# Kernel optimization log

Measured on AMD Instinct MI355X. Metric: run time of the kernel, lower is better.

The kernel has to match this reference:

```python
import jax, jax.numpy as jnp
import numpy as np

EMBED_DIM = 512

def _equalized_linear(x, W):
    # StyleGAN equalized LR: effective weight = W / sqrt(fan_in); out = x @ W_eff.T
    c = 1.0 / np.sqrt(W.shape[1])
    return jnp.einsum('bnd,ed->bne', x, W) * c

def setup_inputs() -> dict:
    key = jax.random.key(0)
    ks = jax.random.split(key, 6)
    B, N, D = 16, 2048, 512
    return {
        'q': jax.random.normal(ks[0], (B, N, D), dtype=jnp.float32),
        'k': jax.random.normal(ks[1], (B, N, D), dtype=jnp.float32),
        'v': jax.random.normal(ks[2], (B, N, D), dtype=jnp.float32),
        'Wq': jax.random.normal(ks[3], (EMBED_DIM, D), dtype=jnp.float32),
        'Wk': jax.random.normal(ks[4], (EMBED_DIM, D), dtype=jnp.float32),
        'Wv': jax.random.normal(ks[5], (EMBED_DIM, D), dtype=jnp.float32),
    }

def reference(q, k, v, Wq, Wk, Wv):
    scale = EMBED_DIM ** (-0.5)
    qp = _equalized_linear(q, Wq)  # [B,Nq,E]
    kp = _equalized_linear(k, Wk)  # [B,Nk,E]
    vp = _equalized_linear(v, Wv)  # [B,Nk,E]
    dots = jnp.einsum('bqe,bke->bqk', qp, kp) * scale  # [B,Nq,Nk]
    attn = jax.nn.softmax(dots, axis=-1)
    out = jnp.einsum('bqk,bke->bqe', attn, vp)  # [B,Nq,E]
    return (out, attn)
```

## Files before the change

kernel.cpp:

```cpp
#include <hip/hip_runtime.h>
#include <hip/hip_bf16.h>

typedef __attribute__((ext_vector_type(8))) short short8;
typedef __attribute__((ext_vector_type(4))) float floatx4;

#define LDP 72
#define TP  136

#define ATTN_OFF ((size_t)16 * 2048 * 512)

__device__ __forceinline__ unsigned short f2bf(float f) {
    union { __hip_bfloat16 h; unsigned short u; } cv;
    cv.h = __float2bfloat16(f);
    return cv.u;
}

__device__ __forceinline__ uint2 f4_to_bf4(float x, float y, float z, float w) {
    uint2 r;
    r.x = (unsigned)f2bf(x) | ((unsigned)f2bf(y) << 16);
    r.y = (unsigned)f2bf(z) | ((unsigned)f2bf(w) << 16);
    return r;
}

__global__ __launch_bounds__(256, 2)
void proj_kernel(const float* __restrict__ q, const float* __restrict__ k,
                 const float* __restrict__ v, const float* __restrict__ wq,
                 const float* __restrict__ wk, const float* __restrict__ wv,
                 unsigned short* __restrict__ qp, unsigned short* __restrict__ kp,
                 unsigned short* __restrict__ vpT)
{
    const int mat = blockIdx.z;
    const float* __restrict__ x = (mat == 0) ? q : (mat == 1) ? k : v;
    const float* __restrict__ w = (mat == 0) ? wq : (mat == 1) ? wk : wv;
    const float scale = (mat == 0) ? (1.0f / 512.0f) : 0.044194173824159216f;

    const int m0 = blockIdx.x * 128;
    const int n0 = blockIdx.y * 128;

    __shared__ __align__(16) unsigned short sm[2 * 128 * LDP];
    unsigned short* lds_a = sm;
    unsigned short* lds_b = sm + 128 * LDP;
    unsigned short* lds_t = sm;

    const int t = threadIdx.x;
    const int wave = t >> 6, ln = t & 15, qd = (t >> 4) & 3;
    const int wm = wave >> 1, wn = wave & 1;

    floatx4 acc[4][4];
    for (int mi = 0; mi < 4; ++mi)
        for (int ni = 0; ni < 4; ++ni)
            acc[mi][ni] = (floatx4){0.f, 0.f, 0.f, 0.f};

    for (int kb = 0; kb < 512; kb += 64) {
        for (int i = 0; i < 8; ++i) {
            int lin = t + 256 * i;
            int row = lin >> 4, c4 = lin & 15;
            const float4 a4 = *(const float4*)&x[(size_t)(m0 + row) * 512 + kb + c4 * 4];
            *(uint2*)&lds_a[row * LDP + c4 * 4] = f4_to_bf4(a4.x, a4.y, a4.z, a4.w);
            const float4 b4 = *(const float4*)&w[(size_t)(n0 + row) * 512 + kb + c4 * 4];
            *(uint2*)&lds_b[row * LDP + c4 * 4] = f4_to_bf4(b4.x, b4.y, b4.z, b4.w);
        }
        __syncthreads();
        for (int kk = 0; kk < 2; ++kk) {
            short8 af[4], bg[4];
            for (int mi = 0; mi < 4; ++mi)
                af[mi] = *(const short8*)&lds_a[(wm * 64 + mi * 16 + ln) * LDP + kk * 32 + qd * 8];
            for (int ni = 0; ni < 4; ++ni)
                bg[ni] = *(const short8*)&lds_b[(wn * 64 + ni * 16 + ln) * LDP + kk * 32 + qd * 8];
            for (int mi = 0; mi < 4; ++mi)
                for (int ni = 0; ni < 4; ++ni)
                    acc[mi][ni] = __builtin_amdgcn_mfma_f32_16x16x32_bf16(
                        af[mi], bg[ni], acc[mi][ni], 0, 0, 0);
        }
        __syncthreads();
    }

    for (int mi = 0; mi < 4; ++mi)
        for (int ni = 0; ni < 4; ++ni)
            for (int r = 0; r < 4; ++r) {
                float val = acc[mi][ni][r] * scale;
                int row = wm * 64 + mi * 16 + qd * 4 + r;
                int col = wn * 64 + ni * 16 + ln;
                if (mat == 2) lds_t[col * TP + row] = f2bf(val);
                else          lds_t[row * TP + col] = f2bf(val);
            }
    __syncthreads();
    if (mat < 2) {
        unsigned short* dst = (mat == 0) ? qp : kp;
        for (int i = 0; i < 8; ++i) {
            int lin = t + 256 * i;
            int row = lin >> 4, c8 = lin & 15;
            *(uint4*)&dst[(size_t)(m0 + row) * 512 + n0 + c8 * 8] =
                *(const uint4*)&lds_t[row * TP + c8 * 8];
        }
    } else {
        int b = m0 >> 11;
        int tloc = m0 & 2047;
        for (int i = 0; i < 8; ++i) {
            int lin = t + 256 * i;
            int row = lin >> 4, c8 = lin & 15;
            *(uint4*)&vpT[(size_t)b * 512 * 2048 + (size_t)(n0 + row) * 2048 + tloc + c8 * 8] =
                *(const uint4*)&lds_t[row * TP + c8 * 8];
        }
    }
}

__global__ __launch_bounds__(256, 2)
void dots_kernel(const unsigned short* __restrict__ qp, const unsigned short* __restrict__ kp,
                 float* __restrict__ attn, float* __restrict__ lsum)
{
    const int b = blockIdx.z;
    const int row0 = blockIdx.y * 128;
    const int col0 = blockIdx.x * 128;

    __shared__ __align__(16) unsigned short sm[2 * 128 * LDP];
    unsigned short* lds_a = sm;
    unsigned short* lds_b = sm + 128 * LDP;
    __shared__ float lds_l[128];

    const int t = threadIdx.x;
    const int wave = t >> 6, ln = t & 15, qd = (t >> 4) & 3;
    const int wm = wave >> 1, wn = wave & 1;

    if (t < 128) lds_l[t] = 0.f;

    const unsigned short* arow = qp + (size_t)(b * 2048 + row0) * 512;
    const unsigned short* brow = kp + (size_t)(b * 2048 + col0) * 512;

    floatx4 acc[4][4];
    for (int mi = 0; mi < 4; ++mi)
        for (int ni = 0; ni < 4; ++ni)
            acc[mi][ni] = (floatx4){0.f, 0.f, 0.f, 0.f};

    for (int kb = 0; kb < 512; kb += 64) {
        for (int i = 0; i < 4; ++i) {
            int lin = t + 256 * i;
            int row = lin >> 3, c8 = lin & 7;
            *(uint4*)&lds_a[row * LDP + c8 * 8] = *(const uint4*)&arow[(size_t)row * 512 + kb + c8 * 8];
            *(uint4*)&lds_b[row * LDP + c8 * 8] = *(const uint4*)&brow[(size_t)row * 512 + kb + c8 * 8];
        }
        __syncthreads();
        for (int kk = 0; kk < 2; ++kk) {
            short8 af[4], bg[4];
            for (int mi = 0; mi < 4; ++mi)
                af[mi] = *(const short8*)&lds_a[(wm * 64 + mi * 16 + ln) * LDP + kk * 32 + qd * 8];
            for (int ni = 0; ni < 4; ++ni)
                bg[ni] = *(const short8*)&lds_b[(wn * 64 + ni * 16 + ln) * LDP + kk * 32 + qd * 8];
            for (int mi = 0; mi < 4; ++mi)
                for (int ni = 0; ni < 4; ++ni)
                    acc[mi][ni] = __builtin_amdgcn_mfma_f32_16x16x32_bf16(
                        af[mi], bg[ni], acc[mi][ni], 0, 0, 0);
        }
        __syncthreads();
    }

    float* attnb = attn + (size_t)(b * 2048 + row0) * 2048 + col0;
    for (int mi = 0; mi < 4; ++mi) {
        float s[4] = {0.f, 0.f, 0.f, 0.f};
        for (int ni = 0; ni < 4; ++ni) {
            int colL = wn * 64 + ni * 16 + ln;
            for (int r = 0; r < 4; ++r) {
                float p = __expf(acc[mi][ni][r]);
                int rowL = wm * 64 + mi * 16 + qd * 4 + r;
                attnb[(size_t)rowL * 2048 + colL] = p;
                s[r] += p;
            }
        }
        for (int r = 0; r < 4; ++r) {
            float vv = s[r];
            vv += __shfl_xor(vv, 1);
            vv += __shfl_xor(vv, 2);
            vv += __shfl_xor(vv, 4);
            vv += __shfl_xor(vv, 8);
            if (ln == 0) atomicAdd(&lds_l[wm * 64 + mi * 16 + qd * 4 + r], vv);
        }
    }
    __syncthreads();
    if (t < 128) atomicAdd(&lsum[b * 2048 + row0 + t], lds_l[t]);
}

__global__ __launch_bounds__(256, 2)
void out_kernel(const unsigned short* __restrict__ vpT, float* __restrict__ attn,
                const float* __restrict__ lsum, float* __restrict__ out)
{
    const int b = blockIdx.y;
    const int row0 = blockIdx.x * 64;

    __shared__ __align__(16) unsigned short p_lds[64 * TP];
    __shared__ __align__(16) unsigned short v_lds[128 * TP];
    __shared__ float inv_l[64];

    const int t = threadIdx.x;
    const int wave = t >> 6, ln = t & 15, qd = (t >> 4) & 3;

    if (t < 64) inv_l[t] = 1.0f / lsum[b * 2048 + row0 + t];

    floatx4 acc[4][8];
    for (int mi = 0; mi < 4; ++mi)
        for (int j = 0; j < 8; ++j)
            acc[mi][j] = (floatx4){0.f, 0.f, 0.f, 0.f};

    float* attnb = attn + (size_t)(b * 2048 + row0) * 2048;
    const unsigned short* vb = vpT + (size_t)b * 512 * 2048;

    for (int kc = 0; kc < 2048; kc += 128) {
        __syncthreads();
        for (int i = 0; i < 8; ++i) {
            int lin = t + 256 * i;
            int row = lin >> 5, c4 = lin & 31;
            float* ad = &attnb[(size_t)row * 2048 + kc + c4 * 4];
            float4 p4 = *(float4*)ad;
            float il = inv_l[row];
            p4.x *= il; p4.y *= il; p4.z *= il; p4.w *= il;
            *(float4*)ad = p4;
            *(uint2*)&p_lds[row * TP + c4 * 4] = f4_to_bf4(p4.x, p4.y, p4.z, p4.w);
        }
        for (int nh = 0; nh < 4; ++nh) {
            __syncthreads();
            for (int i = 0; i < 8; ++i) {
                int lin = t + 256 * i;
                int row = lin >> 4, c8 = lin & 15;
                *(uint4*)&v_lds[row * TP + c8 * 8] =
                    *(const uint4*)&vb[(size_t)(nh * 128 + row) * 2048 + kc + c8 * 8];
            }
            __syncthreads();
            for (int ks = 0; ks < 4; ++ks) {
                short8 af[4];
                for (int mi = 0; mi < 4; ++mi)
                    af[mi] = *(const short8*)&p_lds[(mi * 16 + ln) * TP + ks * 32 + qd * 8];
                for (int ni = 0; ni < 2; ++ni) {
                    short8 bg = *(const short8*)&v_lds[(wave * 32 + ni * 16 + ln) * TP + ks * 32 + qd * 8];
                    for (int mi = 0; mi < 4; ++mi)
                        acc[mi][nh * 2 + ni] = __builtin_amdgcn_mfma_f32_16x16x32_bf16(
                            af[mi], bg, acc[mi][nh * 2 + ni], 0, 0, 0);
                }
            }
        }
    }

    float* outb = out + (size_t)(b * 2048 + row0) * 512;
    for (int mi = 0; mi < 4; ++mi)
        for (int j = 0; j < 8; ++j) {
            int col = (j >> 1) * 128 + wave * 32 + (j & 1) * 16 + ln;
            for (int r = 0; r < 4; ++r) {
                int rowL = mi * 16 + qd * 4 + r;
                outb[(size_t)rowL * 512 + col] = acc[mi][j][r];
            }
        }
}

extern "C" void kernel_launch(void* const* d_in, const int* in_sizes, int n_in,
                              void* d_out, int out_size, void* d_ws, size_t ws_size,
                              hipStream_t stream) {
    const float* q  = (const float*)d_in[0];
    const float* k  = (const float*)d_in[1];
    const float* v  = (const float*)d_in[2];
    const float* wq = (const float*)d_in[3];
    const float* wk = (const float*)d_in[4];
    const float* wv = (const float*)d_in[5];

    unsigned short* qp  = (unsigned short*)d_ws;
    unsigned short* kp  = qp + (size_t)32768 * 512;
    unsigned short* vpT = kp + (size_t)32768 * 512;
    float* lsum = (float*)(vpT + (size_t)16 * 512 * 2048);

    float* out  = (float*)d_out;
    float* attn = out + ATTN_OFF;

    hipMemsetAsync(lsum, 0, (size_t)16 * 2048 * sizeof(float), stream);

    proj_kernel<<<dim3(256, 4, 3), 256, 0, stream>>>(q, k, v, wq, wk, wv, qp, kp, vpT);
    dots_kernel<<<dim3(16, 16, 16), 256, 0, stream>>>(qp, kp, attn, lsum);
    out_kernel<<<dim3(32, 16), 256, 0, stream>>>(vpT, attn, lsum, out);
}
```

Measured before the change: 1.089 ms.

## Restructure out_kernel: 128-row tiles, double-buffered P, direct global V fragments

Rewrites the attn@V kernel to use 512-thread blocks, each covering 128 query rows over all 512 output columns, with an 8-wave 2x4 layout. The normalized P tile is double-buffered in LDS in 32-column steps, and the next step's attention values are prefetched while MFMAs run. V fragments are now loaded straight from global memory into registers instead of being staged through LDS. The aim is to cut LDS traffic and syncs and to overlap the attn read/normalize/write with compute. The risks are uncoalesced global V loads, a barrier every 32 columns, and higher register pressure from 32 accumulators plus 8 B fragments.

```diff
diff --git a/kernel.cpp b/kernel.cpp
--- a/kernel.cpp
+++ b/kernel.cpp
@@ -6,6 +6,7 @@
 
 #define LDP 72
 #define TP  136
+#define PP  40
 
 #define ATTN_OFF ((size_t)16 * 2048 * 512)
 
@@ -179,72 +180,96 @@
     if (t < 128) atomicAdd(&lsum[b * 2048 + row0 + t], lds_l[t]);
 }
 
-__global__ __launch_bounds__(256, 2)
+__global__ __launch_bounds__(512, 2)
 void out_kernel(const unsigned short* __restrict__ vpT, float* __restrict__ attn,
                 const float* __restrict__ lsum, float* __restrict__ out)
 {
-    const int b = blockIdx.y;
-    const int row0 = blockIdx.x * 64;
-
-    __shared__ __align__(16) unsigned short p_lds[64 * TP];
-    __shared__ __align__(16) unsigned short v_lds[128 * TP];
-    __shared__ float inv_l[64];
+    const int b  = blockIdx.x;
+    const int r0 = blockIdx.y * 128;
+
+    __shared__ __align__(16) unsigned short p_lds[2][128 * PP];
 
     const int t = threadIdx.x;
     const int wave = t >> 6, ln = t & 15, qd = (t >> 4) & 3;
-
-    if (t < 64) inv_l[t] = 1.0f / lsum[b * 2048 + row0 + t];
+    const int wm = wave >> 2, wn = wave & 3;
+
+    const int prow = t >> 2;
+    const int pcol = (t & 3) * 8;
+    const float il = 1.0f / lsum[b * 2048 + r0 + prow];
+
+    float* pbase = attn + (size_t)(b * 2048 + r0 + prow) * 2048 + pcol;
+    const unsigned short* vb = vpT + (size_t)b * 512 * 2048;
 
     floatx4 acc[4][8];
-    for (int mi = 0; mi < 4; ++mi)
-        for (int j = 0; j < 8; ++j)
-            acc[mi][j] = (floatx4){0.f, 0.f, 0.f, 0.f};
-
-    float* attnb = attn + (size_t)(b * 2048 + row0) * 2048;
-    const unsigned short* vb = vpT + (size_t)b * 512 * 2048;
-
-    for (int kc = 0; kc < 2048; kc += 128) {
-        __syncthreads();
-        for (int i = 0; i < 8; ++i) {
-            int lin = t + 256 * i;
-            int row = lin >> 5, c4 = lin & 31;
-            float* ad = &attnb[(size_t)row * 2048 + kc + c4 * 4];
-            float4 p4 = *(float4*)ad;
-            float il = inv_l[row];
-            p4.x *= il; p4.y *= il; p4.z *= il; p4.w *= il;
-            *(float4*)ad = p4;
-            *(uint2*)&p_lds[row * TP + c4 * 4] = f4_to_bf4(p4.x, p4.y, p4.z, p4.w);
-        }
-        for (int nh = 0; nh < 4; ++nh) {
-            __syncthreads();
-            for (int i = 0; i < 8; ++i) {
-                int lin = t + 256 * i;
-                int row = lin >> 4, c8 = lin & 15;
-                *(uint4*)&v_lds[row * TP + c8 * 8] =
-                    *(const uint4*)&vb[(size_t)(nh * 128 + row) * 2048 + kc + c8 * 8];
-            }
-            __syncthreads();
-            for (int ks = 0; ks < 4; ++ks) {
-                short8 af[4];
-                for (int mi = 0; mi < 4; ++mi)
-                    af[mi] = *(const short8*)&p_lds[(mi * 16 + ln) * TP + ks * 32 + qd * 8];
-                for (int ni = 0; ni < 2; ++ni) {
-                    short8 bg = *(const short8*)&v_lds[(wave * 32 + ni * 16 + ln) * TP + ks * 32 + qd * 8];
-                    for (int mi = 0; mi < 4; ++mi)
-                        acc[mi][nh * 2 + ni] = __builtin_amdgcn_mfma_f32_16x16x32_bf16(
-                            af[mi], bg, acc[mi][nh * 2 + ni], 0, 0, 0);
-                }
-            }
-        }
-    }
-
-    float* outb = out + (size_t)(b * 2048 + row0) * 512;
-    for (int mi = 0; mi < 4; ++mi)
-        for (int j = 0; j < 8; ++j) {
-            int col = (j >> 1) * 128 + wave * 32 + (j & 1) * 16 + ln;
+    #pragma unroll
+    for (int mi = 0; mi < 4; ++mi)
+        #pragma unroll
+        for (int ni = 0; ni < 8; ++ni)
+            acc[mi][ni] = (floatx4){0.f, 0.f, 0.f, 0.f};
+
+    {
+        float4 pa = *(const float4*)(pbase);
+        float4 pb = *(const float4*)(pbase + 4);
+        pa.x *= il; pa.y *= il; pa.z *= il; pa.w *= il;
+        pb.x *= il; pb.y *= il; pb.z *= il; pb.w *= il;
+        *(float4*)(pbase)     = pa;
+        *(float4*)(pbase + 4) = pb;
+        uint2 lo = f4_to_bf4(pa.x, pa.y, pa.z, pa.w);
+        uint2 hi = f4_to_bf4(pb.x, pb.y, pb.z, pb.w);
+        uint4 pk = {lo.x, lo.y, hi.x, hi.y};
+        *(uint4*)&p_lds[0][prow * PP + pcol] = pk;
+    }
+
+    for (int i = 0; i < 64; ++i) {
+        const int kc = i * 32;
+        const int buf = i & 1;
+        __syncthreads();
+
+        short8 bg[8];
+        #pragma unroll
+        for (int ni = 0; ni < 8; ++ni)
+            bg[ni] = *(const short8*)&vb[(size_t)(wn * 128 + ni * 16 + ln) * 2048 + kc + qd * 8];
+
+        float4 pa, pb;
+        if (i < 63) {
+            pa = *(const float4*)(pbase + kc + 32);
+            pb = *(const float4*)(pbase + kc + 36);
+        }
+
+        short8 af[4];
+        #pragma unroll
+        for (int mi = 0; mi < 4; ++mi)
+            af[mi] = *(const short8*)&p_lds[buf][(wm * 64 + mi * 16 + ln) * PP + qd * 8];
+
+        #pragma unroll
+        for (int ni = 0; ni < 8; ++ni)
+            #pragma unroll
+            for (int mi = 0; mi < 4; ++mi)
+                acc[mi][ni] = __builtin_amdgcn_mfma_f32_16x16x32_bf16(
+                    af[mi], bg[ni], acc[mi][ni], 0, 0, 0);
+
+        if (i < 63) {
+            pa.x *= il; pa.y *= il; pa.z *= il; pa.w *= il;
+            pb.x *= il; pb.y *= il; pb.z *= il; pb.w *= il;
+            *(float4*)(pbase + kc + 32) = pa;
+            *(float4*)(pbase + kc + 36) = pb;
+            uint2 lo = f4_to_bf4(pa.x, pa.y, pa.z, pa.w);
+            uint2 hi = f4_to_bf4(pb.x, pb.y, pb.z, pb.w);
+            uint4 pk = {lo.x, lo.y, hi.x, hi.y};
+            *(uint4*)&p_lds[buf ^ 1][prow * PP + pcol] = pk;
+        }
+    }
+
+    float* outb = out + (size_t)(b * 2048 + r0) * 512;
+    #pragma unroll
+    for (int mi = 0; mi < 4; ++mi)
+        #pragma unroll
+        for (int ni = 0; ni < 8; ++ni) {
+            int col = wn * 128 + ni * 16 + ln;
+            #pragma unroll
             for (int r = 0; r < 4; ++r) {
-                int rowL = mi * 16 + qd * 4 + r;
-                outb[(size_t)rowL * 512 + col] = acc[mi][j][r];
+                int row = wm * 64 + mi * 16 + qd * 4 + r;
+                outb[(size_t)row * 512 + col] = acc[mi][ni][r];
             }
         }
 }
@@ -271,5 +296,5 @@
 
     proj_kernel<<<dim3(256, 4, 3), 256, 0, stream>>>(q, k, v, wq, wk, wv, qp, kp, vpT);
     dots_kernel<<<dim3(16, 16, 16), 256, 0, stream>>>(qp, kp, attn, lsum);
-    out_kernel<<<dim3(32, 16), 256, 0, stream>>>(vpT, attn, lsum, out);
-}
+    out_kernel<<<dim3(16, 16), 512, 0, stream>>>(vpT, attn, lsum, out);
+}
```

After: 917.8 us. 1.19x faster.
